# Kernel optimization log

Measured on AMD Instinct MI355X. Metric: run time of the kernel, lower is better.

The kernel has to match this reference:

```python
import jax, jax.numpy as jnp
import numpy as np

S = 20  # number of standard amino acids; hardcoded in the original layer


def expm_fixed(A, squarings=6, terms=14):
    """Scaling-and-squaring matrix exponential with fixed squaring count.
    A: (..., n, n). tau*Q entries are small (tau ~ softplus(-3)), so a fixed
    2^-6 scaling + Taylor-14 matches tf.linalg.expm to fp32 tolerance."""
    A = A / (2.0 ** squarings)
    I = jnp.broadcast_to(jnp.eye(A.shape[-1], dtype=A.dtype), A.shape)
    out = I
    term = I
    for i in range(1, terms + 1):
        term = jnp.matmul(term, A) / i
        out = out + term
    for _ in range(squarings):
        out = jnp.matmul(out, out)
    return out


def make_rate_matrix(R, p, eps=1e-16):
    """R: (N, s, s) symmetric exchangeabilities, zero diag. p: (N, s) equilibrium."""
    Q = R * p[:, None, :]                       # Q[i,j] = R[i,j] * p[j]
    diag = jnp.sum(Q, axis=-1, keepdims=True)   # (N, s, 1)
    eye = jnp.eye(Q.shape[-1], dtype=Q.dtype)
    Q = Q - diag * eye
    mue = jnp.sum(p[:, :, None] * diag, axis=-2, keepdims=True)  # (N,1,1)
    return Q / jnp.maximum(mue, eps)


def setup_inputs() -> dict:
    key = jax.random.key(0)
    ks = jax.random.split(key, 6)
    m, b, L, k, nr = 2, 256, 1024, 4, 100
    inputs = jax.random.uniform(ks[0], (m, b, L, S), dtype=jnp.float32)
    rate_indices = jax.random.randint(ks[1], (m, b), 0, nr, dtype=jnp.int64)
    # rate_init = constant(-3.0); small jitter so gradients are non-degenerate
    tau_kernel = -3.0 + 0.1 * jax.random.normal(ks[2], (m, nr), dtype=jnp.float32)
    exchangeability_kernel = 0.1 * jax.random.normal(ks[3], (m, k, S, S), dtype=jnp.float32)
    equilibrium_kernel = 0.1 * jax.random.normal(ks[4], (m, k, S), dtype=jnp.float32)
    per_matrix_rates_kernel = 0.1 * jax.random.normal(ks[5], (m, k), dtype=jnp.float32)
    return {
        "inputs": inputs,
        "tau_kernel": tau_kernel,
        "exchangeability_kernel": exchangeability_kernel,
        "equilibrium_kernel": equilibrium_kernel,
        "per_matrix_rates_kernel": per_matrix_rates_kernel,
        "rate_indices": rate_indices,
    }


def reference(inputs, tau_kernel, exchangeability_kernel, equilibrium_kernel,
              per_matrix_rates_kernel, rate_indices):
    m, b, L, s = inputs.shape
    k = exchangeability_kernel.shape[1]
    # make_tau(subset): gather per-sequence times then softplus
    tau = jax.nn.softplus(jnp.take_along_axis(tau_kernel, rate_indices, axis=1))  # (m,b)
    # per-matrix rates
    pmr = jax.nn.softplus(per_matrix_rates_kernel)  # (m,k)
    mut_rates = tau[:, :, None] * pmr[:, None, :]   # (m,b,k)
    # make_R: symmetrize, softplus, zero diagonal
    K = exchangeability_kernel
    R = jax.nn.softplus(0.5 * (K + jnp.swapaxes(K, -1, -2)))
    R = R * (1.0 - jnp.eye(s, dtype=R.dtype))       # (m,k,s,s)
    # make_p
    p = jax.nn.softmax(equilibrium_kernel, axis=-1)  # (m,k,s)
    # normalized rate matrices
    Q = make_rate_matrix(R.reshape(-1, s, s), p.reshape(-1, s)).reshape(m, k, s, s)
    # tau * Q, batched over sequences: (m,b,k,s,s)
    tauQ = mut_rates[..., None, None] * Q[:, None]
    P = expm_fixed(tauQ.reshape(-1, s, s)).reshape(m, b, k, s, s)
    # vector-format inputs path (non-transposed): mbLz,mbkzs->mbLks
    anc = jnp.einsum('mblz,mbkzs->mblks', inputs, P)
    # documented output: (num_model, b, L, num_matrices*s)
    return anc.reshape(m, b, L, k * s)
```

## Files before the change

### kernel.cpp

```cpp
#include <hip/hip_runtime.h>
#include <math.h>

#define M_  2
#define B_  256
#define L_  1024
#define K_  4
#define S_  20
#define NR_ 100
#define NTERM 7

__device__ __forceinline__ float softplusf(float x) {
    return x > 20.0f ? x : log1pf(expf(x));
}

__global__ __launch_bounds__(512)
void qpow_kernel(const float* __restrict__ exch,
                 const float* __restrict__ equil,
                 float*       __restrict__ Qpow)
{
    __shared__ float sQ[400];
    __shared__ float sT[2][400];
    __shared__ float sRow[20];

    const int blk = blockIdx.x;
    const int kk = blk % K_;
    const int mm = blk / K_;
    const int tid = threadIdx.x;
    const bool act = tid < 400;
    const int i = tid / 20;
    const int j = tid - i * 20;

    float p[20];
    float Q0 = 0.0f, rowsum = 0.0f;

    if (act) {
        const float* eq = equil + (mm * K_ + kk) * S_;
        float mx = eq[0];
        #pragma unroll
        for (int z = 1; z < 20; ++z) mx = fmaxf(mx, eq[z]);
        float s = 0.0f;
        #pragma unroll
        for (int z = 0; z < 20; ++z) { p[z] = expf(eq[z] - mx); s += p[z]; }
        const float inv = 1.0f / s;
        #pragma unroll
        for (int z = 0; z < 20; ++z) p[z] *= inv;

        const float* Kx = exch + (mm * K_ + kk) * S_ * S_;
        float R = (i == j) ? 0.0f : softplusf(0.5f * (Kx[i * 20 + j] + Kx[j * 20 + i]));
        Q0 = R * p[j];
        sQ[tid] = Q0;
    }
    __syncthreads();

    if (act) {
        rowsum = 0.0f;
        #pragma unroll
        for (int z = 0; z < 20; ++z) rowsum += sQ[i * 20 + z];
        if (j == 0) sRow[i] = rowsum;
    }
    __syncthreads();

    float* Tout = Qpow + (size_t)blk * (NTERM * 400);
    if (act) {
        float mue = 0.0f;
        #pragma unroll
        for (int z = 0; z < 20; ++z) mue += p[z] * sRow[z];
        float q = (Q0 - ((i == j) ? rowsum : 0.0f)) / fmaxf(mue, 1e-16f);
        sQ[tid] = q;
        sT[0][tid] = q;
        Tout[tid] = q;
    }
    __syncthreads();

    int cur = 0;
    for (int n = 2; n <= NTERM; ++n) {
        if (act) {
            float acc = 0.0f;
            #pragma unroll
            for (int z = 0; z < 20; ++z) acc += sT[cur][i * 20 + z] * sQ[z * 20 + j];
            acc /= (float)n;
            sT[cur ^ 1][tid] = acc;
            Tout[(n - 1) * 400 + tid] = acc;
        }
        __syncthreads();
        cur ^= 1;
    }
}

#define RPB 128
#define TPB 320

__device__ __forceinline__ void fma4(float4& a, float s, const float4& p) {
    a.x = fmaf(s, p.x, a.x);
    a.y = fmaf(s, p.y, a.y);
    a.z = fmaf(s, p.z, a.z);
    a.w = fmaf(s, p.w, a.w);
}

__global__ __launch_bounds__(TPB)
void einsum_kernel(const float* __restrict__ inp,
                   const float* __restrict__ Qpow,
                   const float* __restrict__ tauk,
                   const float* __restrict__ pmrk,
                   const int*   __restrict__ ridx,
                   float*       __restrict__ out)
{
    __shared__ float Pl[K_ * 400];
    __shared__ float inL[RPB * 20];
    __shared__ float sMu[K_];

    const int bx    = blockIdx.x;
    const int chunk = bx & 7;
    const int mb    = bx >> 3;
    const int mm    = mb >> 8;
    const int tid   = threadIdx.x;

    const int r = ridx[mb];

    if (tid < K_) {
        const float tau = softplusf(tauk[mm * NR_ + r]);
        const float pm  = softplusf(pmrk[mm * K_ + tid]);
        sMu[tid] = tau * pm;
    }

    {
        const float4* Isrc = (const float4*)(inp + ((size_t)mb * L_ + chunk * RPB) * 20);
        float4* Id = (float4*)inL;
        for (int idx = tid; idx < RPB * 5; idx += TPB) Id[idx] = Isrc[idx];
    }
    __syncthreads();

    for (int idx = tid; idx < K_ * 400; idx += TPB) {
        const int kk = idx / 400;
        const int el = idx - kk * 400;
        const float* T = Qpow + ((size_t)(mm * K_ + kk) * NTERM) * 400 + el;
        const float mu = sMu[kk];
        float acc = (el % 21 == 0) ? 1.0f : 0.0f;
        float mp = mu;
        #pragma unroll
        for (int n = 0; n < NTERM; ++n) { acc = fmaf(mp, T[n * 400], acc); mp *= mu; }
        Pl[idx] = acc;
    }
    __syncthreads();

    const int t  = tid % 20;
    const int rg = tid / 20;
    const int k  = t / 5;
    const int s0 = (t - k * 5) * 4;
    const float* Pk = Pl + k * 400 + s0;

    float4 acc[8];
    #pragma unroll
    for (int r8 = 0; r8 < 8; ++r8) acc[r8] = make_float4(0.f, 0.f, 0.f, 0.f);

    #pragma unroll
    for (int z4 = 0; z4 < 5; ++z4) {
        const float4 p0 = *(const float4*)(Pk + (z4 * 4 + 0) * 20);
        const float4 p1 = *(const float4*)(Pk + (z4 * 4 + 1) * 20);
        const float4 p2 = *(const float4*)(Pk + (z4 * 4 + 2) * 20);
        const float4 p3 = *(const float4*)(Pk + (z4 * 4 + 3) * 20);
        #pragma unroll
        for (int r8 = 0; r8 < 8; ++r8) {
            const int l = rg + r8 * 16;
            const float4 av = *(const float4*)(inL + l * 20 + z4 * 4);
            fma4(acc[r8], av.x, p0);
            fma4(acc[r8], av.y, p1);
            fma4(acc[r8], av.z, p2);
            fma4(acc[r8], av.w, p3);
        }
    }

    float* ob = out + ((size_t)mb * L_ + chunk * RPB) * 80;
    #pragma unroll
    for (int r8 = 0; r8 < 8; ++r8) {
        const int l = rg + r8 * 16;
        *(float4*)(ob + l * 80 + t * 4) = acc[r8];
    }
}

extern "C" void kernel_launch(void* const* d_in, const int* in_sizes, int n_in,
                              void* d_out, int out_size, void* d_ws, size_t ws_size,
                              hipStream_t stream) {
    const float* inp   = (const float*)d_in[0];
    const float* tauk  = (const float*)d_in[1];
    const float* exch  = (const float*)d_in[2];
    const float* equil = (const float*)d_in[3];
    const float* pmrk  = (const float*)d_in[4];
    const int*   ridx  = (const int*)d_in[5];
    float* outp = (float*)d_out;
    float* Qpow = (float*)d_ws;

    qpow_kernel<<<M_ * K_, 512, 0, stream>>>(exch, equil, Qpow);
    einsum_kernel<<<M_ * B_ * (L_ / RPB), TPB, 0, stream>>>(inp, Qpow, tauk, pmrk, ridx, outp);
}
```

Baseline: 62.77 us.

## Precompute per-rate P matrices in separate kernel and halve einsum row tile

Adds a pbuild kernel that evaluates the truncated Taylor series once for each of the 100 distinct rate indices per model and matrix, writing the P matrices to workspace. The einsum kernel then copies a precomputed 6.4KB P block instead of recomputing the polynomial from the Qpow terms in every block. This removes the redundant per-block series evaluation, which was repeated across 8 chunks per sequence and across sequences sharing a rate index. RPB drops from 128 to 64 and launch bounds ask for 8 blocks per CU, doubling the grid and raising occupancy. The cost is an extra kernel launch and more P traffic per output row.

```diff
diff --git a/kernel.cpp b/kernel.cpp
--- a/kernel.cpp
+++ b/kernel.cpp
@@ -87,7 +87,30 @@
     }
 }
 
-#define RPB 128
+__global__ __launch_bounds__(512)
+void pbuild_kernel(const float* __restrict__ Qpow,
+                   const float* __restrict__ tauk,
+                   const float* __restrict__ pmrk,
+                   float*       __restrict__ Pws)
+{
+    const int blk = blockIdx.x;
+    const int kk = blk % K_;
+    const int rr = (blk / K_) % NR_;
+    const int mm = blk / (K_ * NR_);
+    const int tid = threadIdx.x;
+    if (tid >= 400) return;
+
+    const float mu = softplusf(tauk[mm * NR_ + rr]) * softplusf(pmrk[mm * K_ + kk]);
+    const float* T = Qpow + ((size_t)(mm * K_ + kk) * NTERM) * 400 + tid;
+
+    float acc = (tid % 21 == 0) ? 1.0f : 0.0f;
+    float mp = mu;
+    #pragma unroll
+    for (int n = 0; n < NTERM; ++n) { acc = fmaf(mp, T[n * 400], acc); mp *= mu; }
+    Pws[(size_t)blk * 400 + tid] = acc;
+}
+
+#define RPB 64
 #define TPB 320
 
 __device__ __forceinline__ void fma4(float4& a, float s, const float4& p) {
@@ -97,49 +120,31 @@
     a.w = fmaf(s, p.w, a.w);
 }
 
-__global__ __launch_bounds__(TPB)
+__global__ __launch_bounds__(TPB, 8)
 void einsum_kernel(const float* __restrict__ inp,
-                   const float* __restrict__ Qpow,
-                   const float* __restrict__ tauk,
-                   const float* __restrict__ pmrk,
+                   const float* __restrict__ Pws,
                    const int*   __restrict__ ridx,
                    float*       __restrict__ out)
 {
     __shared__ float Pl[K_ * 400];
     __shared__ float inL[RPB * 20];
-    __shared__ float sMu[K_];
 
     const int bx    = blockIdx.x;
-    const int chunk = bx & 7;
-    const int mb    = bx >> 3;
+    const int chunk = bx & 15;
+    const int mb    = bx >> 4;
     const int mm    = mb >> 8;
     const int tid   = threadIdx.x;
 
     const int r = ridx[mb];
 
-    if (tid < K_) {
-        const float tau = softplusf(tauk[mm * NR_ + r]);
-        const float pm  = softplusf(pmrk[mm * K_ + tid]);
-        sMu[tid] = tau * pm;
-    }
-
     {
+        const float4* Psrc = (const float4*)(Pws + ((size_t)(mm * NR_ + r) * K_) * 400);
+        float4* Pd = (float4*)Pl;
+        Pd[tid] = Psrc[tid];
+        if (tid < 80) Pd[320 + tid] = Psrc[320 + tid];
+
         const float4* Isrc = (const float4*)(inp + ((size_t)mb * L_ + chunk * RPB) * 20);
-        float4* Id = (float4*)inL;
-        for (int idx = tid; idx < RPB * 5; idx += TPB) Id[idx] = Isrc[idx];
-    }
-    __syncthreads();
-
-    for (int idx = tid; idx < K_ * 400; idx += TPB) {
-        const int kk = idx / 400;
-        const int el = idx - kk * 400;
-        const float* T = Qpow + ((size_t)(mm * K_ + kk) * NTERM) * 400 + el;
-        const float mu = sMu[kk];
-        float acc = (el % 21 == 0) ? 1.0f : 0.0f;
-        float mp = mu;
-        #pragma unroll
-        for (int n = 0; n < NTERM; ++n) { acc = fmaf(mp, T[n * 400], acc); mp *= mu; }
-        Pl[idx] = acc;
+        ((float4*)inL)[tid] = Isrc[tid];
     }
     __syncthreads();
 
@@ -149,9 +154,9 @@
     const int s0 = (t - k * 5) * 4;
     const float* Pk = Pl + k * 400 + s0;
 
-    float4 acc[8];
-    #pragma unroll
-    for (int r8 = 0; r8 < 8; ++r8) acc[r8] = make_float4(0.f, 0.f, 0.f, 0.f);
+    float4 acc[4];
+    #pragma unroll
+    for (int r4 = 0; r4 < 4; ++r4) acc[r4] = make_float4(0.f, 0.f, 0.f, 0.f);
 
     #pragma unroll
     for (int z4 = 0; z4 < 5; ++z4) {
@@ -160,21 +165,21 @@
         const float4 p2 = *(const float4*)(Pk + (z4 * 4 + 2) * 20);
         const float4 p3 = *(const float4*)(Pk + (z4 * 4 + 3) * 20);
         #pragma unroll
-        for (int r8 = 0; r8 < 8; ++r8) {
-            const int l = rg + r8 * 16;
+        for (int r4 = 0; r4 < 4; ++r4) {
+            const int l = rg + r4 * 16;
             const float4 av = *(const float4*)(inL + l * 20 + z4 * 4);
-            fma4(acc[r8], av.x, p0);
-            fma4(acc[r8], av.y, p1);
-            fma4(acc[r8], av.z, p2);
-            fma4(acc[r8], av.w, p3);
+            fma4(acc[r4], av.x, p0);
+            fma4(acc[r4], av.y, p1);
+            fma4(acc[r4], av.z, p2);
+            fma4(acc[r4], av.w, p3);
         }
     }
 
     float* ob = out + ((size_t)mb * L_ + chunk * RPB) * 80;
     #pragma unroll
-    for (int r8 = 0; r8 < 8; ++r8) {
-        const int l = rg + r8 * 16;
-        *(float4*)(ob + l * 80 + t * 4) = acc[r8];
+    for (int r4 = 0; r4 < 4; ++r4) {
+        const int l = rg + r4 * 16;
+        *(float4*)(ob + l * 80 + t * 4) = acc[r4];
     }
 }
 
@@ -188,8 +193,11 @@
     const float* pmrk  = (const float*)d_in[4];
     const int*   ridx  = (const int*)d_in[5];
     float* outp = (float*)d_out;
+
     float* Qpow = (float*)d_ws;
+    float* Pws  = Qpow + (size_t)M_ * K_ * NTERM * 400;
 
     qpow_kernel<<<M_ * K_, 512, 0, stream>>>(exch, equil, Qpow);
-    einsum_kernel<<<M_ * B_ * (L_ / RPB), TPB, 0, stream>>>(inp, Qpow, tauk, pmrk, ridx, outp);
-}
+    pbuild_kernel<<<M_ * NR_ * K_, 512, 0, stream>>>(Qpow, tauk, pmrk, Pws);
+    einsum_kernel<<<M_ * B_ * (L_ / RPB), TPB, 0, stream>>>(inp, Pws, ridx, outp);
+}
```

Result: slower. 126.1 us (+100.8%).
